# Optimization experiments

Hardware: AMD Instinct MI355X
Metric: run time of the kernel (lower is better)

The kernel has to match this reference:

```python
import jax, jax.numpy as jnp
import numpy as np

N = 4096      # batch size
D = 512       # flattened feature dim
C = 128       # num classes / output dim
K = 2         # knn k (module default)
ALPHA = 0.0005


def _safe_sqrt(d2):
    # sqrt with zero (not nan) gradient at exactly 0, matching torch.norm
    d2 = jnp.maximum(d2, 0.0)
    safe = jnp.where(d2 > 0, d2, 1.0)
    return jnp.where(d2 > 0, jnp.sqrt(safe), 0.0)


def _pairwise_dist(a):
    # a: [n, d] -> [n, n] euclidean distances via gram trick
    sq = jnp.sum(a * a, axis=1)
    d2 = sq[:, None] + sq[None, :] - 2.0 * (a @ a.T)
    return _safe_sqrt(d2)


def setup_inputs() -> dict:
    key = jax.random.key(0)
    k1, k2, k3, k4 = jax.random.split(key, 4)
    x_batch = jax.random.normal(k1, (N, D), jnp.float32)
    y_batch = jax.random.randint(k2, (N,), 0, C)
    y_output = jax.random.normal(k3, (N, C), jnp.float32)
    W = jax.random.normal(k4, (D, C), jnp.float32) * 0.02
    b = jnp.zeros((C,), jnp.float32)
    return {"x_batch": x_batch, "y_batch": y_batch, "y_output": y_output, "W": W, "b": b}


def reference(x_batch, y_batch, y_output, W, b):
    n = x_batch.shape[0]
    # ---- loss_function(net(x_batch), y_batch): linear net + cross entropy ----
    logits = x_batch.reshape(n, -1) @ W + b                     # [n, C]
    logp = jax.nn.log_softmax(logits, axis=-1)
    loss = -jnp.mean(jnp.take_along_axis(logp, y_batch[:, None], axis=1))

    # ---- compute_weights_based_on_knn (vectorized) ----
    dx = _pairwise_dist(x_batch.reshape(n, -1))                 # [n, n]
    order = jnp.argsort(dx, axis=1)                             # sklearn kneighbors order
    d_sorted = jnp.take_along_axis(dx, order, axis=1)           # sorted distances (sklearn d)
    e_d = jnp.exp(-d_sorted)                                    # [n, n]
    nbr = order[:, :K + 1]                                      # [n, K+1] raw indices
    rows = jnp.arange(n)[:, None]
    nbr_mask = jnp.zeros((n, n), jnp.float32).at[rows, nbr].set(1.0)  # j in neighbors[i]
    same = (y_batch[:, None] == y_batch[None, :]).astype(jnp.float32)
    # w_diff = w_int - 0; w_int[i,j] = e_d[i,j] (raw-j index into sorted e_d, as in source)
    w_diff = e_d * nbr_mask * same                              # [n, n]

    # ---- weighted_output: sum_ij ||y_out[i]-y_out[j]|| * w_diff[i,j] ----
    dy = _pairwise_dist(y_output)                               # [n, n]
    reg = jnp.sum(dy * w_diff)

    return loss + ALPHA * reg
```

## Files before the change

### kernel.cpp

```cpp
#include <hip/hip_runtime.h>
#include <math.h>
#include <stdint.h>

#define N 4096
#define D 512
#define C 128
#define ALPHA 0.0005f
#define NT_TILES 32
#define TRI (NT_TILES * (NT_TILES + 1) / 2)
#define NBLK (TRI + N / 128)

typedef __bf16 bf16x8 __attribute__((ext_vector_type(8)));
typedef float f32x4 __attribute__((ext_vector_type(4)));

__global__ __launch_bounds__(256) void prep_kernel(const float* __restrict__ x,
                                                   float* __restrict__ sq,
                                                   float* __restrict__ dot0,
                                                   __bf16* __restrict__ xb,
                                                   const float* __restrict__ W,
                                                   __bf16* __restrict__ Wtb,
                                                   unsigned* __restrict__ cnt) {
    if (blockIdx.x >= N) {
        const int tid = (blockIdx.x - N) * 256 + threadIdx.x;
        const int k = tid >> 7;
        const int n = tid & 127;
        Wtb[(size_t)n * D + k] = (__bf16)W[tid];
        return;
    }
    const int i = blockIdx.x;
    const int t = threadIdx.x;
    if (t == 0) cnt[i] = 0u;
    float s1 = 0.f, s2 = 0.f;
    for (int k = t; k < D; k += 256) {
        float v = x[(size_t)i * D + k];
        xb[(size_t)i * D + k] = (__bf16)v;
        s1 += v * v;
        s2 += v * x[k];
    }
    for (int o = 32; o; o >>= 1) {
        s1 += __shfl_down(s1, o);
        s2 += __shfl_down(s2, o);
    }
    __shared__ float r1[4], r2[4];
    if ((t & 63) == 0) { r1[t >> 6] = s1; r2[t >> 6] = s2; }
    __syncthreads();
    if (t == 0) {
        sq[i]   = r1[0] + r1[1] + r1[2] + r1[3];
        dot0[i] = r2[0] + r2[1] + r2[2] + r2[3];
    }
}

__global__ __launch_bounds__(256) void fused_mfma(const __bf16* __restrict__ xb,
                                                  const __bf16* __restrict__ Wtb,
                                                  const float* __restrict__ sq,
                                                  const float* __restrict__ dot0,
                                                  const int* __restrict__ y,
                                                  const float* __restrict__ b,
                                                  unsigned* __restrict__ cnt,
                                                  float* __restrict__ lossrow) {
    __shared__ __bf16 Alds[2][128 * 32];
    __shared__ __bf16 Blds[2][128 * 32];
    __shared__ float rmax[128][2];
    __shared__ float rsum[128][2];
    const int t = threadIdx.x;
    const int w = t >> 6, l = t & 63;
    const int wy = w >> 1, wx = w & 1;
    const int kg = l >> 4, lr = l & 15;

    const int bid = (int)blockIdx.x;
    const bool isCE = (bid >= TRI);
    int bi, bj;
    bool diag = false;
    const __bf16* Bbase;
    if (isCE) {
        bi = (bid - TRI) * 128;
        bj = 0;
        Bbase = Wtb;
    } else {
        int tj = (int)((sqrtf(8.f * (float)bid + 1.f) - 1.f) * 0.5f);
        while (tj * (tj + 1) / 2 > bid) --tj;
        while ((tj + 1) * (tj + 2) / 2 <= bid) ++tj;
        const int ti = bid - tj * (tj + 1) / 2;
        bi = ti * 128;
        bj = tj * 128;
        diag = (ti == tj);
        Bbase = xb + (size_t)bj * D;
    }
    const __bf16* Abase = xb + (size_t)bi * D;

    f32x4 acc[4][4];
    const f32x4 zero = {0.f, 0.f, 0.f, 0.f};
#pragma unroll
    for (int mt = 0; mt < 4; ++mt)
#pragma unroll
        for (int nt = 0; nt < 4; ++nt) acc[mt][nt] = zero;

    const int e0 = t, e1 = t + 256;
    const int r0 = e0 >> 2, c0 = e0 & 3;
    const int r1 = e1 >> 2, c1 = e1 & 3;
    const int sc0 = (c0 ^ (r0 & 3) ^ ((r0 >> 2) & 3)) & 3;
    const int sc1 = (c1 ^ (r1 & 3) ^ ((r1 >> 2) & 3)) & 3;

    const __bf16* Ap0 = Abase + (size_t)r0 * D + sc0 * 8;
    const __bf16* Ap1 = Abase + (size_t)r1 * D + sc1 * 8;
    const __bf16* Bp0 = Bbase + (size_t)r0 * D + sc0 * 8;
    const __bf16* Bp1 = Bbase + (size_t)r1 * D + sc1 * 8;

    uint4 ra0 = *(const uint4*)Ap0;
    uint4 ra1 = *(const uint4*)Ap1;
    uint4 rb0, rb1;
    if (!diag) { rb0 = *(const uint4*)Bp0; rb1 = *(const uint4*)Bp1; }

    for (int k = 0; k < 16; ++k) {
        const int buf = k & 1;
        *(uint4*)((char*)Alds[buf] + e0 * 16) = ra0;
        *(uint4*)((char*)Alds[buf] + e1 * 16) = ra1;
        if (!diag) {
            *(uint4*)((char*)Blds[buf] + e0 * 16) = rb0;
            *(uint4*)((char*)Blds[buf] + e1 * 16) = rb1;
        }
        if (k < 15) {
            const int off = (k + 1) * 32;
            ra0 = *(const uint4*)(Ap0 + off);
            ra1 = *(const uint4*)(Ap1 + off);
            if (!diag) {
                rb0 = *(const uint4*)(Bp0 + off);
                rb1 = *(const uint4*)(Bp1 + off);
            }
        }
        __syncthreads();
        const __bf16* Al = Alds[buf];
        const __bf16* Bl = diag ? Alds[buf] : Blds[buf];
        bf16x8 av[4], bv[4];
#pragma unroll
        for (int mt = 0; mt < 4; ++mt) {
            const int row = wy * 64 + mt * 16 + lr;
            const int slot = (kg ^ (row & 3) ^ ((row >> 2) & 3)) & 3;
            av[mt] = *(const bf16x8*)(Al + row * 32 + slot * 8);
        }
#pragma unroll
        for (int nt = 0; nt < 4; ++nt) {
            const int row = wx * 64 + nt * 16 + lr;
            const int slot = (kg ^ (row & 3) ^ ((row >> 2) & 3)) & 3;
            bv[nt] = *(const bf16x8*)(Bl + row * 32 + slot * 8);
        }
#pragma unroll
        for (int mt = 0; mt < 4; ++mt)
#pragma unroll
            for (int nt = 0; nt < 4; ++nt)
                acc[mt][nt] = __builtin_amdgcn_mfma_f32_16x16x32_bf16(av[mt], bv[nt], acc[mt][nt], 0, 0, 0);
    }

    if (isCE) {
        int jn[4]; float bb[4];
#pragma unroll
        for (int nt = 0; nt < 4; ++nt) { jn[nt] = wx * 64 + nt * 16 + lr; bb[nt] = b[jn[nt]]; }
#pragma unroll
        for (int mt = 0; mt < 4; ++mt)
#pragma unroll
            for (int r = 0; r < 4; ++r) {
                float m = acc[mt][0][r] + bb[0];
#pragma unroll
                for (int nt = 1; nt < 4; ++nt) m = fmaxf(m, acc[mt][nt][r] + bb[nt]);
                m = fmaxf(m, __shfl_xor(m, 1));
                m = fmaxf(m, __shfl_xor(m, 2));
                m = fmaxf(m, __shfl_xor(m, 4));
                m = fmaxf(m, __shfl_xor(m, 8));
                if (lr == 0) rmax[wy * 64 + mt * 16 + kg * 4 + r][wx] = m;
            }
        __syncthreads();
        float mrow[4][4];
#pragma unroll
        for (int mt = 0; mt < 4; ++mt)
#pragma unroll
            for (int r = 0; r < 4; ++r) {
                const int ri = wy * 64 + mt * 16 + kg * 4 + r;
                mrow[mt][r] = fmaxf(rmax[ri][0], rmax[ri][1]);
                float s = 0.f;
#pragma unroll
                for (int nt = 0; nt < 4; ++nt) s += expf(acc[mt][nt][r] + bb[nt] - mrow[mt][r]);
                s += __shfl_xor(s, 1);
                s += __shfl_xor(s, 2);
                s += __shfl_xor(s, 4);
                s += __shfl_xor(s, 8);
                if (lr == 0) rsum[ri][wx] = s;
            }
        __syncthreads();
#pragma unroll
        for (int mt = 0; mt < 4; ++mt)
#pragma unroll
            for (int r = 0; r < 4; ++r) {
                const int ri = wy * 64 + mt * 16 + kg * 4 + r;
                const int i = bi + ri;
                const float s = rsum[ri][0] + rsum[ri][1];
                const int yi = y[i];
#pragma unroll
                for (int nt = 0; nt < 4; ++nt)
                    if (jn[nt] == yi)
                        lossrow[i] = -(acc[mt][nt][r] + bb[nt] - mrow[mt][r] - logf(s));
            }
    } else {
        const float sq0 = sq[0];
        int jn[4]; float sqj[4], thrj[4];
#pragma unroll
        for (int nt = 0; nt < 4; ++nt) {
            jn[nt] = bj + wx * 64 + nt * 16 + lr;
            sqj[nt] = sq[jn[nt]];
            thrj[nt] = sq0 - 2.0f * dot0[jn[nt]];
        }
        unsigned cj[4] = {0u, 0u, 0u, 0u};
#pragma unroll
        for (int mt = 0; mt < 4; ++mt)
#pragma unroll
            for (int r = 0; r < 4; ++r) {
                const int i = bi + wy * 64 + mt * 16 + kg * 4 + r;
                const float thri = sq0 - 2.0f * dot0[i];
                const float sqi = sq[i];
                unsigned ci = 0;
                if (diag) {
#pragma unroll
                    for (int nt = 0; nt < 4; ++nt) {
                        const float d = acc[mt][nt][r];
                        const int j = jn[nt];
                        if (sqj[nt] - 2.0f * d < thri && j != i && j != 0) ++ci;
                    }
                } else {
#pragma unroll
                    for (int nt = 0; nt < 4; ++nt) {
                        const float d = acc[mt][nt][r];
                        if (sqj[nt] - 2.0f * d < thri) ++ci;
                        if (sqi - 2.0f * d < thrj[nt] && i != 0) ++cj[nt];
                    }
                }
                ci += __shfl_xor((int)ci, 1);
                ci += __shfl_xor((int)ci, 2);
                ci += __shfl_xor((int)ci, 4);
                ci += __shfl_xor((int)ci, 8);
                if (lr == 0 && ci) atomicAdd(&cnt[i], ci);
            }
        if (!diag) {
#pragma unroll
            for (int nt = 0; nt < 4; ++nt) {
                unsigned v = cj[nt];
                v += __shfl_xor((int)v, 16);
                v += __shfl_xor((int)v, 32);
                if (l < 16 && v) atomicAdd(&cnt[jn[nt]], v);
            }
        }
    }
}

__global__ __launch_bounds__(256) void final_kernel(const float* __restrict__ lossrow,
                                                    const unsigned* __restrict__ cnt,
                                                    const int* __restrict__ y,
                                                    const float* __restrict__ Y,
                                                    float* __restrict__ out) {
    const int t = threadIdx.x;
    const int y0 = y[0];
    double ls = 0.0, rs = 0.0;
    for (int i = t; i < N; i += 256) {
        ls += (double)lossrow[i];
        if (i > 0 && y[i] == y0 && cnt[i] <= 1u) {
            float d2 = 0.f;
            for (int c = 0; c < C; ++c) {
                float d = Y[(size_t)i * C + c] - Y[c];
                d2 += d * d;
            }
            rs += (double)sqrtf(fmaxf(d2, 0.f));
        }
    }
    for (int o = 32; o; o >>= 1) {
        ls += __shfl_down(ls, o);
        rs += __shfl_down(rs, o);
    }
    __shared__ double dl[4], dr[4];
    if ((t & 63) == 0) { dl[t >> 6] = ls; dr[t >> 6] = rs; }
    __syncthreads();
    if (t == 0) {
        double L = (dl[0] + dl[1] + dl[2] + dl[3]) / (double)N;
        double R = (dr[0] + dr[1] + dr[2] + dr[3]);
        out[0] = (float)(L + (double)ALPHA * R);
    }
}

extern "C" void kernel_launch(void* const* d_in, const int* in_sizes, int n_in,
                              void* d_out, int out_size, void* d_ws, size_t ws_size,
                              hipStream_t stream) {
    const float* x  = (const float*)d_in[0];
    const int*   y  = (const int*)d_in[1];
    const float* Y  = (const float*)d_in[2];
    const float* W  = (const float*)d_in[3];
    const float* b  = (const float*)d_in[4];
    float* out = (float*)d_out;

    float* wsf      = (float*)d_ws;
    float* lossrow  = wsf;
    float* sq       = wsf + N;
    float* dot0     = wsf + 2 * N;
    unsigned* cnt   = (unsigned*)(wsf + 3 * N);
    __bf16* xb      = (__bf16*)(wsf + 4 * N);
    __bf16* Wtb     = (__bf16*)((char*)xb + (size_t)N * D * 2);

    prep_kernel<<<N + (D * C) / 256, 256, 0, stream>>>(x, sq, dot0, xb, W, Wtb, cnt);
    fused_mfma<<<NBLK, 256, 0, stream>>>(xb, Wtb, sq, dot0, y, b, cnt, lossrow);
    final_kernel<<<1, 256, 0, stream>>>(lossrow, cnt, y, Y, out);
}
```

Measured before the change: 117.0 us.

## Use persistent atomic work queue for fused MFMA tiles and vectorize prep

The fused GEMM kernel becomes persistent: a fixed grid of 1024 blocks pulls tile indices from a global atomic counter instead of launching one block per tile. The prep kernel now handles one row per wavefront with float4 loads and a packed bf16 store, which drops the LDS reduction. The final reduction runs with 1024 threads, and the LDS barrier is replaced by an inline s_waitcnt lgkmcnt plus s_barrier. The queue adds an atomic and a __syncthreads per tile, and the relaxed barrier depends on the global loads not needing a vmcnt wait.

```diff
diff --git a/kernel.cpp b/kernel.cpp
--- a/kernel.cpp
+++ b/kernel.cpp
@@ -8,10 +8,15 @@
 #define ALPHA 0.0005f
 #define NT_TILES 32
 #define TRI (NT_TILES * (NT_TILES + 1) / 2)
-#define NBLK (TRI + N / 128)
+#define NTILE (TRI + N / 128)
+#define GRID_FUSED 1024
 
 typedef __bf16 bf16x8 __attribute__((ext_vector_type(8)));
 typedef float f32x4 __attribute__((ext_vector_type(4)));
+
+__device__ __forceinline__ void wg_barrier_lgkm() {
+    asm volatile("s_waitcnt lgkmcnt(0)\n\ts_barrier" ::: "memory");
+}
 
 __global__ __launch_bounds__(256) void prep_kernel(const float* __restrict__ x,
                                                    float* __restrict__ sq,
@@ -19,35 +24,36 @@
                                                    __bf16* __restrict__ xb,
                                                    const float* __restrict__ W,
                                                    __bf16* __restrict__ Wtb,
-                                                   unsigned* __restrict__ cnt) {
-    if (blockIdx.x >= N) {
-        const int tid = (blockIdx.x - N) * 256 + threadIdx.x;
+                                                   unsigned* __restrict__ cnt,
+                                                   unsigned* __restrict__ qhead) {
+    if (blockIdx.x >= N / 4) {
+        const int tid = (blockIdx.x - N / 4) * 256 + threadIdx.x;
         const int k = tid >> 7;
         const int n = tid & 127;
         Wtb[(size_t)n * D + k] = (__bf16)W[tid];
+        if (blockIdx.x == N / 4 && threadIdx.x == 0) *qhead = 0u;
         return;
     }
-    const int i = blockIdx.x;
-    const int t = threadIdx.x;
-    if (t == 0) cnt[i] = 0u;
-    float s1 = 0.f, s2 = 0.f;
-    for (int k = t; k < D; k += 256) {
-        float v = x[(size_t)i * D + k];
-        xb[(size_t)i * D + k] = (__bf16)v;
-        s1 += v * v;
-        s2 += v * x[k];
-    }
-    for (int o = 32; o; o >>= 1) {
-        s1 += __shfl_down(s1, o);
-        s2 += __shfl_down(s2, o);
-    }
-    __shared__ float r1[4], r2[4];
-    if ((t & 63) == 0) { r1[t >> 6] = s1; r2[t >> 6] = s2; }
-    __syncthreads();
-    if (t == 0) {
-        sq[i]   = r1[0] + r1[1] + r1[2] + r1[3];
-        dot0[i] = r2[0] + r2[1] + r2[2] + r2[3];
-    }
+    const int i = blockIdx.x * 4 + (threadIdx.x >> 6);
+    const int l = threadIdx.x & 63;
+    const float* xp = x + (size_t)i * D + l * 8;
+    const float4 v0 = *(const float4*)(xp);
+    const float4 v1 = *(const float4*)(xp + 4);
+    const float4 u0 = *(const float4*)(x + l * 8);
+    const float4 u1 = *(const float4*)(x + l * 8 + 4);
+    float s1 = v0.x * v0.x + v0.y * v0.y + v0.z * v0.z + v0.w * v0.w
+             + v1.x * v1.x + v1.y * v1.y + v1.z * v1.z + v1.w * v1.w;
+    float s2 = v0.x * u0.x + v0.y * u0.y + v0.z * u0.z + v0.w * u0.w
+             + v1.x * u1.x + v1.y * u1.y + v1.z * u1.z + v1.w * u1.w;
+    bf16x8 o;
+    o[0] = (__bf16)v0.x; o[1] = (__bf16)v0.y; o[2] = (__bf16)v0.z; o[3] = (__bf16)v0.w;
+    o[4] = (__bf16)v1.x; o[5] = (__bf16)v1.y; o[6] = (__bf16)v1.z; o[7] = (__bf16)v1.w;
+    *(bf16x8*)(xb + (size_t)i * D + l * 8) = o;
+    for (int off = 32; off; off >>= 1) {
+        s1 += __shfl_down(s1, off);
+        s2 += __shfl_down(s2, off);
+    }
+    if (l == 0) { sq[i] = s1; dot0[i] = s2; cnt[i] = 0u; }
 }
 
 __global__ __launch_bounds__(256) void fused_mfma(const __bf16* __restrict__ xb,
@@ -57,43 +63,17 @@
                                                   const int* __restrict__ y,
                                                   const float* __restrict__ b,
                                                   unsigned* __restrict__ cnt,
-                                                  float* __restrict__ lossrow) {
+                                                  float* __restrict__ lossrow,
+                                                  unsigned* __restrict__ qhead) {
     __shared__ __bf16 Alds[2][128 * 32];
     __shared__ __bf16 Blds[2][128 * 32];
     __shared__ float rmax[128][2];
     __shared__ float rsum[128][2];
+    __shared__ int bidS;
     const int t = threadIdx.x;
     const int w = t >> 6, l = t & 63;
     const int wy = w >> 1, wx = w & 1;
     const int kg = l >> 4, lr = l & 15;
-
-    const int bid = (int)blockIdx.x;
-    const bool isCE = (bid >= TRI);
-    int bi, bj;
-    bool diag = false;
-    const __bf16* Bbase;
-    if (isCE) {
-        bi = (bid - TRI) * 128;
-        bj = 0;
-        Bbase = Wtb;
-    } else {
-        int tj = (int)((sqrtf(8.f * (float)bid + 1.f) - 1.f) * 0.5f);
-        while (tj * (tj + 1) / 2 > bid) --tj;
-        while ((tj + 1) * (tj + 2) / 2 <= bid) ++tj;
-        const int ti = bid - tj * (tj + 1) / 2;
-        bi = ti * 128;
-        bj = tj * 128;
-        diag = (ti == tj);
-        Bbase = xb + (size_t)bj * D;
-    }
-    const __bf16* Abase = xb + (size_t)bi * D;
-
-    f32x4 acc[4][4];
-    const f32x4 zero = {0.f, 0.f, 0.f, 0.f};
-#pragma unroll
-    for (int mt = 0; mt < 4; ++mt)
-#pragma unroll
-        for (int nt = 0; nt < 4; ++nt) acc[mt][nt] = zero;
 
     const int e0 = t, e1 = t + 256;
     const int r0 = e0 >> 2, c0 = e0 & 3;
@@ -101,164 +81,198 @@
     const int sc0 = (c0 ^ (r0 & 3) ^ ((r0 >> 2) & 3)) & 3;
     const int sc1 = (c1 ^ (r1 & 3) ^ ((r1 >> 2) & 3)) & 3;
 
-    const __bf16* Ap0 = Abase + (size_t)r0 * D + sc0 * 8;
-    const __bf16* Ap1 = Abase + (size_t)r1 * D + sc1 * 8;
-    const __bf16* Bp0 = Bbase + (size_t)r0 * D + sc0 * 8;
-    const __bf16* Bp1 = Bbase + (size_t)r1 * D + sc1 * 8;
-
-    uint4 ra0 = *(const uint4*)Ap0;
-    uint4 ra1 = *(const uint4*)Ap1;
-    uint4 rb0, rb1;
-    if (!diag) { rb0 = *(const uint4*)Bp0; rb1 = *(const uint4*)Bp1; }
-
-    for (int k = 0; k < 16; ++k) {
-        const int buf = k & 1;
-        *(uint4*)((char*)Alds[buf] + e0 * 16) = ra0;
-        *(uint4*)((char*)Alds[buf] + e1 * 16) = ra1;
-        if (!diag) {
-            *(uint4*)((char*)Blds[buf] + e0 * 16) = rb0;
-            *(uint4*)((char*)Blds[buf] + e1 * 16) = rb1;
+    for (;;) {
+        if (t == 0) bidS = (int)atomicAdd(qhead, 1u);
+        __syncthreads();
+        const int bid = bidS;
+        if (bid >= NTILE) break;
+
+        const bool isCE = (bid >= TRI);
+        int bi, bj;
+        bool diag = false;
+        const __bf16* Bbase;
+        if (isCE) {
+            bi = (bid - TRI) * 128;
+            bj = 0;
+            Bbase = Wtb;
+        } else {
+            int tj = (int)((sqrtf(8.f * (float)bid + 1.f) - 1.f) * 0.5f);
+            while (tj * (tj + 1) / 2 > bid) --tj;
+            while ((tj + 1) * (tj + 2) / 2 <= bid) ++tj;
+            const int ti = bid - tj * (tj + 1) / 2;
+            bi = ti * 128;
+            bj = tj * 128;
+            diag = (ti == tj);
+            Bbase = xb + (size_t)bj * D;
         }
-        if (k < 15) {
-            const int off = (k + 1) * 32;
-            ra0 = *(const uint4*)(Ap0 + off);
-            ra1 = *(const uint4*)(Ap1 + off);
+        const __bf16* Abase = xb + (size_t)bi * D;
+
+        f32x4 acc[4][4];
+        const f32x4 zero = {0.f, 0.f, 0.f, 0.f};
+#pragma unroll
+        for (int mt = 0; mt < 4; ++mt)
+#pragma unroll
+            for (int nt = 0; nt < 4; ++nt) acc[mt][nt] = zero;
+
+        const __bf16* Ap0 = Abase + (size_t)r0 * D + sc0 * 8;
+        const __bf16* Ap1 = Abase + (size_t)r1 * D + sc1 * 8;
+        const __bf16* Bp0 = Bbase + (size_t)r0 * D + sc0 * 8;
+        const __bf16* Bp1 = Bbase + (size_t)r1 * D + sc1 * 8;
+
+        uint4 ra0 = *(const uint4*)Ap0;
+        uint4 ra1 = *(const uint4*)Ap1;
+        uint4 rb0, rb1;
+        if (!diag) { rb0 = *(const uint4*)Bp0; rb1 = *(const uint4*)Bp1; }
+
+        for (int k = 0; k < 16; ++k) {
+            const int buf = k & 1;
+            *(uint4*)((char*)Alds[buf] + e0 * 16) = ra0;
+            *(uint4*)((char*)Alds[buf] + e1 * 16) = ra1;
             if (!diag) {
-                rb0 = *(const uint4*)(Bp0 + off);
-                rb1 = *(const uint4*)(Bp1 + off);
-            }
+                *(uint4*)((char*)Blds[buf] + e0 * 16) = rb0;
+                *(uint4*)((char*)Blds[buf] + e1 * 16) = rb1;
+            }
+            if (k < 15) {
+                const int off = (k + 1) * 32;
+                ra0 = *(const uint4*)(Ap0 + off);
+                ra1 = *(const uint4*)(Ap1 + off);
+                if (!diag) {
+                    rb0 = *(const uint4*)(Bp0 + off);
+                    rb1 = *(const uint4*)(Bp1 + off);
+                }
+            }
+            wg_barrier_lgkm();
+            const __bf16* Al = Alds[buf];
+            const __bf16* Bl = diag ? Alds[buf] : Blds[buf];
+            bf16x8 av[4], bv[4];
+#pragma unroll
+            for (int mt = 0; mt < 4; ++mt) {
+                const int row = wy * 64 + mt * 16 + lr;
+                const int slot = (kg ^ (row & 3) ^ ((row >> 2) & 3)) & 3;
+                av[mt] = *(const bf16x8*)(Al + row * 32 + slot * 8);
+            }
+#pragma unroll
+            for (int nt = 0; nt < 4; ++nt) {
+                const int row = wx * 64 + nt * 16 + lr;
+                const int slot = (kg ^ (row & 3) ^ ((row >> 2) & 3)) & 3;
+                bv[nt] = *(const bf16x8*)(Bl + row * 32 + slot * 8);
+            }
+#pragma unroll
+            for (int mt = 0; mt < 4; ++mt)
+#pragma unroll
+                for (int nt = 0; nt < 4; ++nt)
+                    acc[mt][nt] = __builtin_amdgcn_mfma_f32_16x16x32_bf16(av[mt], bv[nt], acc[mt][nt], 0, 0, 0);
         }
-        __syncthreads();
-        const __bf16* Al = Alds[buf];
-        const __bf16* Bl = diag ? Alds[buf] : Blds[buf];
-        bf16x8 av[4], bv[4];
-#pragma unroll
-        for (int mt = 0; mt < 4; ++mt) {
-            const int row = wy * 64 + mt * 16 + lr;
-            const int slot = (kg ^ (row & 3) ^ ((row >> 2) & 3)) & 3;
-            av[mt] = *(const bf16x8*)(Al + row * 32 + slot * 8);
+
+        if (isCE) {
+            int jn[4]; float bb[4];
+#pragma unroll
+            for (int nt = 0; nt < 4; ++nt) { jn[nt] = wx * 64 + nt * 16 + lr; bb[nt] = b[jn[nt]]; }
+#pragma unroll
+            for (int mt = 0; mt < 4; ++mt)
+#pragma unroll
+                for (int r = 0; r < 4; ++r) {
+                    float m = acc[mt][0][r] + bb[0];
+#pragma unroll
+                    for (int nt = 1; nt < 4; ++nt) m = fmaxf(m, acc[mt][nt][r] + bb[nt]);
+                    m = fmaxf(m, __shfl_xor(m, 1));
+                    m = fmaxf(m, __shfl_xor(m, 2));
+                    m = fmaxf(m, __shfl_xor(m, 4));
+                    m = fmaxf(m, __shfl_xor(m, 8));
+                    if (lr == 0) rmax[wy * 64 + mt * 16 + kg * 4 + r][wx] = m;
+                }
+            __syncthreads();
+            float mrow[4][4];
+#pragma unroll
+            for (int mt = 0; mt < 4; ++mt)
+#pragma unroll
+                for (int r = 0; r < 4; ++r) {
+                    const int ri = wy * 64 + mt * 16 + kg * 4 + r;
+                    mrow[mt][r] = fmaxf(rmax[ri][0], rmax[ri][1]);
+                    float s = 0.f;
+#pragma unroll
+                    for (int nt = 0; nt < 4; ++nt) s += expf(acc[mt][nt][r] + bb[nt] - mrow[mt][r]);
+                    s += __shfl_xor(s, 1);
+                    s += __shfl_xor(s, 2);
+                    s += __shfl_xor(s, 4);
+                    s += __shfl_xor(s, 8);
+                    if (lr == 0) rsum[ri][wx] = s;
+                }
+            __syncthreads();
+#pragma unroll
+            for (int mt = 0; mt < 4; ++mt)
+#pragma unroll
+                for (int r = 0; r < 4; ++r) {
+                    const int ri = wy * 64 + mt * 16 + kg * 4 + r;
+                    const int i = bi + ri;
+                    const float s = rsum[ri][0] + rsum[ri][1];
+                    const int yi = y[i];
+#pragma unroll
+                    for (int nt = 0; nt < 4; ++nt)
+                        if (jn[nt] == yi)
+                            lossrow[i] = -(acc[mt][nt][r] + bb[nt] - mrow[mt][r] - logf(s));
+                }
+        } else {
+            const float sq0 = sq[0];
+            int jn[4]; float sqj[4], thrj[4];
+#pragma unroll
+            for (int nt = 0; nt < 4; ++nt) {
+                jn[nt] = bj + wx * 64 + nt * 16 + lr;
+                sqj[nt] = sq[jn[nt]];
+                thrj[nt] = sq0 - 2.0f * dot0[jn[nt]];
+            }
+            unsigned cj[4] = {0u, 0u, 0u, 0u};
+#pragma unroll
+            for (int mt = 0; mt < 4; ++mt)
+#pragma unroll
+                for (int r = 0; r < 4; ++r) {
+                    const int i = bi + wy * 64 + mt * 16 + kg * 4 + r;
+                    const float thri = sq0 - 2.0f * dot0[i];
+                    const float sqi = sq[i];
+                    unsigned ci = 0;
+                    if (diag) {
+#pragma unroll
+                        for (int nt = 0; nt < 4; ++nt) {
+                            const float d = acc[mt][nt][r];
+                            const int j = jn[nt];
+                            if (sqj[nt] - 2.0f * d < thri && j != i && j != 0) ++ci;
+                        }
+                    } else {
+#pragma unroll
+                        for (int nt = 0; nt < 4; ++nt) {
+                            const float d = acc[mt][nt][r];
+                            if (sqj[nt] - 2.0f * d < thri) ++ci;
+                            if (sqi - 2.0f * d < thrj[nt] && i != 0) ++cj[nt];
+                        }
+                    }
+                    ci += __shfl_xor((int)ci, 1);
+                    ci += __shfl_xor((int)ci, 2);
+                    ci += __shfl_xor((int)ci, 4);
+                    ci += __shfl_xor((int)ci, 8);
+                    if (lr == 0 && ci) atomicAdd(&cnt[i], ci);
+                }
+            if (!diag) {
+#pragma unroll
+                for (int nt = 0; nt < 4; ++nt) {
+                    unsigned v = cj[nt];
+                    v += __shfl_xor((int)v, 16);
+                    v += __shfl_xor((int)v, 32);
+                    if (l < 16 && v) atomicAdd(&cnt[jn[nt]], v);
+                }
+            }
         }
-#pragma unroll
-        for (int nt = 0; nt < 4; ++nt) {
-            const int row = wx * 64 + nt * 16 + lr;
-            const int slot = (kg ^ (row & 3) ^ ((row >> 2) & 3)) & 3;
-            bv[nt] = *(const bf16x8*)(Bl + row * 32 + slot * 8);
-        }
-#pragma unroll
-        for (int mt = 0; mt < 4; ++mt)
-#pragma unroll
-            for (int nt = 0; nt < 4; ++nt)
-                acc[mt][nt] = __builtin_amdgcn_mfma_f32_16x16x32_bf16(av[mt], bv[nt], acc[mt][nt], 0, 0, 0);
-    }
-
-    if (isCE) {
-        int jn[4]; float bb[4];
-#pragma unroll
-        for (int nt = 0; nt < 4; ++nt) { jn[nt] = wx * 64 + nt * 16 + lr; bb[nt] = b[jn[nt]]; }
-#pragma unroll
-        for (int mt = 0; mt < 4; ++mt)
-#pragma unroll
-            for (int r = 0; r < 4; ++r) {
-                float m = acc[mt][0][r] + bb[0];
-#pragma unroll
-                for (int nt = 1; nt < 4; ++nt) m = fmaxf(m, acc[mt][nt][r] + bb[nt]);
-                m = fmaxf(m, __shfl_xor(m, 1));
-                m = fmaxf(m, __shfl_xor(m, 2));
-                m = fmaxf(m, __shfl_xor(m, 4));
-                m = fmaxf(m, __shfl_xor(m, 8));
-                if (lr == 0) rmax[wy * 64 + mt * 16 + kg * 4 + r][wx] = m;
-            }
-        __syncthreads();
-        float mrow[4][4];
-#pragma unroll
-        for (int mt = 0; mt < 4; ++mt)
-#pragma unroll
-            for (int r = 0; r < 4; ++r) {
-                const int ri = wy * 64 + mt * 16 + kg * 4 + r;
-                mrow[mt][r] = fmaxf(rmax[ri][0], rmax[ri][1]);
-                float s = 0.f;
-#pragma unroll
-                for (int nt = 0; nt < 4; ++nt) s += expf(acc[mt][nt][r] + bb[nt] - mrow[mt][r]);
-                s += __shfl_xor(s, 1);
-                s += __shfl_xor(s, 2);
-                s += __shfl_xor(s, 4);
-                s += __shfl_xor(s, 8);
-                if (lr == 0) rsum[ri][wx] = s;
-            }
-        __syncthreads();
-#pragma unroll
-        for (int mt = 0; mt < 4; ++mt)
-#pragma unroll
-            for (int r = 0; r < 4; ++r) {
-                const int ri = wy * 64 + mt * 16 + kg * 4 + r;
-                const int i = bi + ri;
-                const float s = rsum[ri][0] + rsum[ri][1];
-                const int yi = y[i];
-#pragma unroll
-                for (int nt = 0; nt < 4; ++nt)
-                    if (jn[nt] == yi)
-                        lossrow[i] = -(acc[mt][nt][r] + bb[nt] - mrow[mt][r] - logf(s));
-            }
-    } else {
-        const float sq0 = sq[0];
-        int jn[4]; float sqj[4], thrj[4];
-#pragma unroll
-        for (int nt = 0; nt < 4; ++nt) {
-            jn[nt] = bj + wx * 64 + nt * 16 + lr;
-            sqj[nt] = sq[jn[nt]];
-            thrj[nt] = sq0 - 2.0f * dot0[jn[nt]];
-        }
-        unsigned cj[4] = {0u, 0u, 0u, 0u};
-#pragma unroll
-        for (int mt = 0; mt < 4; ++mt)
-#pragma unroll
-            for (int r = 0; r < 4; ++r) {
-                const int i = bi + wy * 64 + mt * 16 + kg * 4 + r;
-                const float thri = sq0 - 2.0f * dot0[i];
-                const float sqi = sq[i];
-                unsigned ci = 0;
-                if (diag) {
-#pragma unroll
-                    for (int nt = 0; nt < 4; ++nt) {
-                        const float d = acc[mt][nt][r];
-                        const int j = jn[nt];
-                        if (sqj[nt] - 2.0f * d < thri && j != i && j != 0) ++ci;
-                    }
-                } else {
-#pragma unroll
-                    for (int nt = 0; nt < 4; ++nt) {
-                        const float d = acc[mt][nt][r];
-                        if (sqj[nt] - 2.0f * d < thri) ++ci;
-                        if (sqi - 2.0f * d < thrj[nt] && i != 0) ++cj[nt];
-                    }
-                }
-                ci += __shfl_xor((int)ci, 1);
-                ci += __shfl_xor((int)ci, 2);
-                ci += __shfl_xor((int)ci, 4);
-                ci += __shfl_xor((int)ci, 8);
-                if (lr == 0 && ci) atomicAdd(&cnt[i], ci);
-            }
-        if (!diag) {
-#pragma unroll
-            for (int nt = 0; nt < 4; ++nt) {
-                unsigned v = cj[nt];
-                v += __shfl_xor((int)v, 16);
-                v += __shfl_xor((int)v, 32);
-                if (l < 16 && v) atomicAdd(&cnt[jn[nt]], v);
-            }
-        }
-    }
-}
-
-__global__ __launch_bounds__(256) void final_kernel(const float* __restrict__ lossrow,
-                                                    const unsigned* __restrict__ cnt,
-                                                    const int* __restrict__ y,
-                                                    const float* __restrict__ Y,
-                                                    float* __restrict__ out) {
+    }
+}
+
+__global__ __launch_bounds__(1024) void final_kernel(const float* __restrict__ lossrow,
+                                                     const unsigned* __restrict__ cnt,
+                                                     const int* __restrict__ y,
+                                                     const float* __restrict__ Y,
+                                                     float* __restrict__ out) {
     const int t = threadIdx.x;
     const int y0 = y[0];
     double ls = 0.0, rs = 0.0;
-    for (int i = t; i < N; i += 256) {
+    for (int i = t; i < N; i += 1024) {
         ls += (double)lossrow[i];
         if (i > 0 && y[i] == y0 && cnt[i] <= 1u) {
             float d2 = 0.f;
@@ -273,13 +287,13 @@
         ls += __shfl_down(ls, o);
         rs += __shfl_down(rs, o);
     }
-    __shared__ double dl[4], dr[4];
+    __shared__ double dl[16], dr[16];
     if ((t & 63) == 0) { dl[t >> 6] = ls; dr[t >> 6] = rs; }
     __syncthreads();
     if (t == 0) {
-        double L = (dl[0] + dl[1] + dl[2] + dl[3]) / (double)N;
-        double R = (dr[0] + dr[1] + dr[2] + dr[3]);
-        out[0] = (float)(L + (double)ALPHA * R);
+        double L = 0.0, R = 0.0;
+        for (int k = 0; k < 16; ++k) { L += dl[k]; R += dr[k]; }
+        out[0] = (float)(L / (double)N + (double)ALPHA * R);
     }
 }
 
@@ -300,8 +314,9 @@
     unsigned* cnt   = (unsigned*)(wsf + 3 * N);
     __bf16* xb      = (__bf16*)(wsf + 4 * N);
     __bf16* Wtb     = (__bf16*)((char*)xb + (size_t)N * D * 2);
-
-    prep_kernel<<<N + (D * C) / 256, 256, 0, stream>>>(x, sq, dot0, xb, W, Wtb, cnt);
-    fused_mfma<<<NBLK, 256, 0, stream>>>(xb, Wtb, sq, dot0, y, b, cnt, lossrow);
-    final_kernel<<<1, 256, 0, stream>>>(lossrow, cnt, y, Y, out);
-}
+    unsigned* qhead = (unsigned*)((char*)Wtb + (size_t)C * D * 2);
+
+    prep_kernel<<<N / 4 + 256, 256, 0, stream>>>(x, sq, dot0, xb, W, Wtb, cnt, qhead);
+    fused_mfma<<<GRID_FUSED, 256, 0, stream>>>(xb, Wtb, sq, dot0, y, b, cnt, lossrow, qhead);
+    final_kernel<<<1, 1024, 0, stream>>>(lossrow, cnt, y, Y, out);
+}
```

Measured after the change: 119.1 us. No clear change (+1.8%).
